# Kernel optimization log

Measured on AMD Instinct MI355X. Metric: run time of the kernel, lower is better.

## Reference

```python
import jax, jax.numpy as jnp
import numpy as np

N = 65536          # flattened batch of latent vectors
D = 64             # latent_dim
K = 1024           # codebook_size


def setup_inputs() -> dict:
    key = jax.random.key(0)
    k1, k2 = jax.random.split(key)
    x = jax.random.normal(k1, (N, D), dtype=jnp.float32)
    # codebook init: uniform(-1/K, 1/K) as in the torch module
    W = jax.random.uniform(k2, (K, D), dtype=jnp.float32,
                           minval=-1.0 / K, maxval=1.0 / K)
    return {"x": x, "W": W}


def reference(x, W):
    L2 = jnp.sum(x * x, axis=1, keepdims=True)          # [N, 1]
    C2 = jnp.sum(W * W, axis=1)[None, :]                # [1, K]
    CL = x @ W.T                                        # [N, K]
    distances = L2 - 2.0 * CL + C2
    closest = jnp.argmin(distances, axis=-1)            # [N] int
    # gather nearest codebook vectors (equivalent to one-hot @ W)
    quantized = W[closest]                              # [N, D]
    return quantized, closest
```

## Files before the change

kernel.cpp:

```cpp
#include <hip/hip_runtime.h>
#include <math.h>

#define NROWS 65536
#define DDIM  64
#define KCB   1024

__global__ void __launch_bounds__(256, 2)
vq_fused_kernel(const float* __restrict__ x, const float* __restrict__ W,
                float* __restrict__ outq, float* __restrict__ outi) {
    __shared__ float c2s[KCB];
    __shared__ float s_bd[4][64];
    __shared__ int   s_bi[4][64];

    const int lane = threadIdx.x & 63;
    const int s    = __builtin_amdgcn_readfirstlane(threadIdx.x >> 6);
    const int row  = blockIdx.x * 64 + lane;

    const float* xr = x + (size_t)row * DDIM;
    float xv[64];
#pragma unroll
    for (int k = 0; k < 64; k += 4) {
        float4 v = *(const float4*)(xr + k);
        xv[k] = v.x; xv[k + 1] = v.y; xv[k + 2] = v.z; xv[k + 3] = v.w;
    }

    {
        const int jbase = threadIdx.x * 4;
#pragma unroll
        for (int c = 0; c < 4; ++c) {
            const float* w = W + (size_t)(jbase + c) * DDIM;
            float r[8];
#pragma unroll
            for (int m = 0; m < 8; ++m) r[m] = __fmul_rn(w[m], w[m]);
#pragma unroll
            for (int i = 8; i < 64; i += 8) {
#pragma unroll
                for (int m = 0; m < 8; ++m)
                    r[m] = __fadd_rn(r[m], __fmul_rn(w[i + m], w[i + m]));
            }
            c2s[jbase + c] = __fadd_rn(
                __fadd_rn(__fadd_rn(r[0], r[1]), __fadd_rn(r[2], r[3])),
                __fadd_rn(__fadd_rn(r[4], r[5]), __fadd_rn(r[6], r[7])));
        }
    }

    float r[8];
#pragma unroll
    for (int m = 0; m < 8; ++m) r[m] = __fmul_rn(xv[m], xv[m]);
#pragma unroll
    for (int i = 8; i < 64; i += 8) {
#pragma unroll
        for (int m = 0; m < 8; ++m)
            r[m] = __fadd_rn(r[m], __fmul_rn(xv[i + m], xv[i + m]));
    }
    const float L2 = __fadd_rn(
        __fadd_rn(__fadd_rn(r[0], r[1]), __fadd_rn(r[2], r[3])),
        __fadd_rn(__fadd_rn(r[4], r[5]), __fadd_rn(r[6], r[7])));

    __syncthreads();

    const int j0 = s * 256;
    float best = INFINITY;
    int   bidx = j0;
    for (int jj = 0; jj < 256; jj += 2) {
        const int j = j0 + jj;
        const float* w0 = W + (size_t)j * DDIM;
        float acc0 = 0.0f, acc1 = 0.0f;
#pragma unroll
        for (int k = 0; k < 64; ++k) {
            acc0 = __builtin_fmaf(xv[k], w0[k], acc0);
            acc1 = __builtin_fmaf(xv[k], w0[DDIM + k], acc1);
        }
        const float d0 = __fadd_rn(__fsub_rn(L2, __fmul_rn(2.0f, acc0)), c2s[j]);
        const float d1 = __fadd_rn(__fsub_rn(L2, __fmul_rn(2.0f, acc1)), c2s[j + 1]);
        if (d0 < best) { best = d0; bidx = j; }
        if (d1 < best) { best = d1; bidx = j + 1; }
    }

    s_bd[s][lane] = best;
    s_bi[s][lane] = bidx;
    __syncthreads();

    if (s == 0) {
        float b  = s_bd[0][lane];
        int   bi = s_bi[0][lane];
#pragma unroll
        for (int t = 1; t < 4; ++t) {
            const float d = s_bd[t][lane];
            if (d < b) { b = d; bi = s_bi[t][lane]; }
        }
        outi[row] = (float)bi;
        s_bi[0][lane] = bi;
    }
    __syncthreads();

    {
        const int t     = threadIdx.x;
        const int rloc  = t >> 2;
        const int quart = t & 3;
        const int j     = s_bi[0][rloc];
        const float* src = W + (size_t)j * DDIM + quart * 16;
        float* dst = outq + ((size_t)blockIdx.x * 64 + rloc) * DDIM + quart * 16;
#pragma unroll
        for (int u = 0; u < 4; ++u)
            *(float4*)(dst + 4 * u) = *(const float4*)(src + 4 * u);
    }
}

extern "C" void kernel_launch(void* const* d_in, const int* in_sizes, int n_in,
                              void* d_out, int out_size, void* d_ws, size_t ws_size,
                              hipStream_t stream) {
    const float* x = (const float*)d_in[0];
    const float* W = (const float*)d_in[1];

    float* outq = (float*)d_out;
    float* outi = (float*)d_out + (size_t)NROWS * DDIM;

    hipLaunchKernelGGL(vq_fused_kernel, dim3(NROWS / 64), dim3(256), 0, stream,
                       x, W, outq, outi);
}
```

Measured before the change: 272.9 us.

## Stage codebook chunks in LDS with register prefetch instead of global reads

```diff
diff --git a/kernel.cpp b/kernel.cpp
--- a/kernel.cpp
+++ b/kernel.cpp
@@ -4,16 +4,21 @@
 #define NROWS 65536
 #define DDIM  64
 #define KCB   1024
+#define CHUNK 64
+#define NCHUNK (KCB / CHUNK)
+#define CHUNK_FLOATS (CHUNK * DDIM)
 
-__global__ void __launch_bounds__(256, 2)
+__global__ void __launch_bounds__(256, 4)
 vq_fused_kernel(const float* __restrict__ x, const float* __restrict__ W,
                 float* __restrict__ outq, float* __restrict__ outi) {
+    __shared__ float wchunk[CHUNK_FLOATS];
     __shared__ float c2s[KCB];
     __shared__ float s_bd[4][64];
     __shared__ int   s_bi[4][64];
 
-    const int lane = threadIdx.x & 63;
-    const int s    = __builtin_amdgcn_readfirstlane(threadIdx.x >> 6);
+    const int tid  = threadIdx.x;
+    const int lane = tid & 63;
+    const int s    = __builtin_amdgcn_readfirstlane(tid >> 6);
     const int row  = blockIdx.x * 64 + lane;
 
     const float* xr = x + (size_t)row * DDIM;
@@ -25,7 +30,7 @@
     }
 
     {
-        const int jbase = threadIdx.x * 4;
+        const int jbase = tid * 4;
 #pragma unroll
         for (int c = 0; c < 4; ++c) {
             const float* w = W + (size_t)(jbase + c) * DDIM;
@@ -57,24 +62,43 @@
         __fadd_rn(__fadd_rn(r[0], r[1]), __fadd_rn(r[2], r[3])),
         __fadd_rn(__fadd_rn(r[4], r[5]), __fadd_rn(r[6], r[7])));
 
-    __syncthreads();
+    float best = INFINITY;
+    int   bidx = 0;
 
-    const int j0 = s * 256;
-    float best = INFINITY;
-    int   bidx = j0;
-    for (int jj = 0; jj < 256; jj += 2) {
-        const int j = j0 + jj;
-        const float* w0 = W + (size_t)j * DDIM;
-        float acc0 = 0.0f, acc1 = 0.0f;
+    float4 pf[4];
 #pragma unroll
-        for (int k = 0; k < 64; ++k) {
-            acc0 = __builtin_fmaf(xv[k], w0[k], acc0);
-            acc1 = __builtin_fmaf(xv[k], w0[DDIM + k], acc1);
+    for (int n = 0; n < 4; ++n)
+        pf[n] = *(const float4*)(W + (size_t)n * 1024 + tid * 4);
+
+    for (int c = 0; c < NCHUNK; ++c) {
+        __syncthreads();
+#pragma unroll
+        for (int n = 0; n < 4; ++n)
+            *(float4*)(&wchunk[n * 1024 + tid * 4]) = pf[n];
+        if (c < NCHUNK - 1) {
+#pragma unroll
+            for (int n = 0; n < 4; ++n)
+                pf[n] = *(const float4*)(W + (size_t)(c + 1) * CHUNK_FLOATS
+                                           + (size_t)n * 1024 + tid * 4);
         }
-        const float d0 = __fadd_rn(__fsub_rn(L2, __fmul_rn(2.0f, acc0)), c2s[j]);
-        const float d1 = __fadd_rn(__fsub_rn(L2, __fmul_rn(2.0f, acc1)), c2s[j + 1]);
-        if (d0 < best) { best = d0; bidx = j; }
-        if (d1 < best) { best = d1; bidx = j + 1; }
+        __syncthreads();
+
+        const int jg0 = c * CHUNK + s * 16;
+        const float* wl = &wchunk[s * 16 * DDIM];
+        for (int p = 0; p < 8; ++p) {
+            const float* w0 = wl + (size_t)(2 * p) * DDIM;
+            float acc0 = 0.0f, acc1 = 0.0f;
+#pragma unroll
+            for (int k = 0; k < 64; ++k) {
+                acc0 = __builtin_fmaf(xv[k], w0[k], acc0);
+                acc1 = __builtin_fmaf(xv[k], w0[DDIM + k], acc1);
+            }
+            const int j = jg0 + 2 * p;
+            const float d0 = __fadd_rn(__fsub_rn(L2, __fmul_rn(2.0f, acc0)), c2s[j]);
+            const float d1 = __fadd_rn(__fsub_rn(L2, __fmul_rn(2.0f, acc1)), c2s[j + 1]);
+            if (d0 < best) { best = d0; bidx = j; }
+            if (d1 < best) { best = d1; bidx = j + 1; }
+        }
     }
 
     s_bd[s][lane] = best;
@@ -87,7 +111,8 @@
 #pragma unroll
         for (int t = 1; t < 4; ++t) {
             const float d = s_bd[t][lane];
-            if (d < b) { b = d; bi = s_bi[t][lane]; }
+            const int   i = s_bi[t][lane];
+            if (d < b || (d == b && i < bi)) { b = d; bi = i; }
         }
         outi[row] = (float)bi;
         s_bi[0][lane] = bi;
@@ -95,9 +120,8 @@
     __syncthreads();
 
     {
-        const int t     = threadIdx.x;
-        const int rloc  = t >> 2;
-        const int quart = t & 3;
+        const int rloc  = tid >> 2;
+        const int quart = tid & 3;
         const int j     = s_bi[0][rloc];
         const float* src = W + (size_t)j * DDIM + quart * 16;
         float* dst = outq + ((size_t)blockIdx.x * 64 + rloc) * DDIM + quart * 16;
```

After: 264.7 us. 1.03x faster.
